# Optimization experiments

Measured on AMD Instinct MI355X. Metric: run time of the kernel, lower is better.

## Reference

```python
import jax, jax.numpy as jnp
import numpy as np

D_MODEL = 1024
NUM_HEADS = 16
DEPTH = D_MODEL // NUM_HEADS


def setup_inputs() -> dict:
    key = jax.random.key(0)
    ks = jax.random.split(key, 6)
    B, S = 2, 2048
    scale = 1.0 / np.sqrt(D_MODEL)
    return {
        "q": jax.random.normal(ks[0], (B, S, D_MODEL), jnp.float32),
        "k": jax.random.normal(ks[1], (B, S, D_MODEL), jnp.float32),
        "v": jax.random.normal(ks[2], (B, S, D_MODEL), jnp.float32),
        "wq": jax.random.normal(ks[3], (D_MODEL, D_MODEL), jnp.float32) * scale,
        "wk": jax.random.normal(ks[4], (D_MODEL, D_MODEL), jnp.float32) * scale,
        "wv": jax.random.normal(ks[5], (D_MODEL, D_MODEL), jnp.float32) * scale,
    }


def reference(q, k, v, wq, wk, wv):
    B, S, _ = q.shape
    # Linear projections (nn.Linear: x @ W.T), then split heads -> [B,H,S,depth]
    def split(x):
        return x.reshape(B, -1, NUM_HEADS, DEPTH).transpose(0, 2, 1, 3)
    Q = split(q @ wq.T)
    K = split(k @ wk.T)
    V = split(v @ wv.T)
    scores = jnp.einsum("bhqd,bhkd->bhqk", Q, K) / np.sqrt(DEPTH).astype(np.float32)
    attn = jax.nn.softmax(scores, axis=-1)
    out = jnp.einsum("bhqk,bhkd->bhqd", attn, V)
    # merge heads; note: original forward never applies self.dense
    return out.transpose(0, 2, 1, 3).reshape(B, S, D_MODEL)
```

## Files before the change

### kernel.cpp

```cpp
#include <hip/hip_runtime.h>
#include <hip/hip_bf16.h>
#include <stdint.h>

#define B_SZ 2
#define S_LEN 2048
#define DM 1024
#define NH 16
#define DEPTH 64
#define M_ROWS (B_SZ * S_LEN)
#define SCALE_Q 0.1803368801111144f

typedef __attribute__((ext_vector_type(8))) short bf16x8;
typedef __attribute__((ext_vector_type(4))) float f32x4;
typedef __attribute__((ext_vector_type(16))) float f32x16;

__device__ __forceinline__ unsigned short f2bf(float x) {
    union { float f; unsigned u; } a; a.f = x;
    unsigned r = a.u + 0x7FFF + ((a.u >> 16) & 1);
    return (unsigned short)(r >> 16);
}

__device__ __forceinline__ bf16x8 u4_to_bf8(uint4 u) {
    union { uint4 a; bf16x8 b; } c; c.a = u; return c.b;
}

__device__ __forceinline__ unsigned cvtpk_bf16(float lo, float hi) {
    unsigned r;
    asm("v_cvt_pk_bf16_f32 %0, %1, %2" : "=v"(r) : "v"(lo), "v"(hi));
    return r;
}

__device__ __forceinline__ void permswap32(unsigned &a, unsigned &b) {
    auto r = __builtin_amdgcn_permlane32_swap(a, b, false, false);
    a = r[0]; b = r[1];
}

__device__ __forceinline__ void async_ld16(const unsigned short* g, void* l) {
    __builtin_amdgcn_global_load_lds(
        (const __attribute__((address_space(1))) void*)g,
        (__attribute__((address_space(3))) void*)l,
        16, 0, 0);
}


__global__ __launch_bounds__(256)
void convert_kernel(const float* __restrict__ q, const float* __restrict__ k,
                    const float* __restrict__ v, const float* __restrict__ wq,
                    const float* __restrict__ wk, const float* __restrict__ wv,
                    unsigned short* __restrict__ dst) {
    const int z = blockIdx.y;
    const float* src = (z == 0) ? q : (z == 1) ? k : (z == 2) ? v
                     : (z == 3) ? wq : (z == 4) ? wk : wv;
    const size_t n4  = (z < 3) ? ((size_t)M_ROWS * DM / 4) : ((size_t)DM * DM / 4);
    const size_t off = (z < 3) ? ((size_t)z * M_ROWS * DM)
                               : ((size_t)3 * M_ROWS * DM + (size_t)(z - 3) * DM * DM);
    unsigned short* d = dst + off;
    const size_t stride = (size_t)gridDim.x * blockDim.x;
    for (size_t i = (size_t)blockIdx.x * blockDim.x + threadIdx.x; i < n4; i += stride) {
        float4 x = ((const float4*)src)[i];
        ushort4 p;
        p.x = f2bf(x.x); p.y = f2bf(x.y); p.z = f2bf(x.z); p.w = f2bf(x.w);
        ((ushort4*)d)[i] = p;
    }
}

__global__ __launch_bounds__(256)
void proj_gemm3_kernel(const unsigned short* __restrict__ Xall,
                       const unsigned short* __restrict__ Wall,
                       unsigned short* __restrict__ Call,
                       unsigned short* __restrict__ Vtp) {
    __shared__ unsigned short SMEM[4 * 128 * 64];

    const int z = blockIdx.z;
    const unsigned short* X = Xall + (size_t)z * M_ROWS * DM;
    const unsigned short* W = Wall + (size_t)z * DM * DM;
    unsigned short* C = Call + (size_t)z * M_ROWS * DM;

    const int tid  = threadIdx.x;
    const int wave = tid >> 6;
    const int lane = tid & 63;
    const int l32  = lane & 31;
    const int s    = lane >> 5;
    const int m0 = blockIdx.x * 128;
    const int n0 = blockIdx.y * 128;
    const int wm = (wave >> 1) * 64;
    const int wn = (wave & 1) * 64;

    const int r8 = lane >> 3;
    const int sc = (lane & 7) ^ r8;

    f32x16 acc[2][2];
#pragma unroll
    for (int mi = 0; mi < 2; ++mi)
#pragma unroll
        for (int ni = 0; ni < 2; ++ni)
#pragma unroll
            for (int r = 0; r < 16; ++r) acc[mi][ni][r] = 0.f;

#pragma unroll
    for (int i = 0; i < 4; ++i) {
        const int r = i * 32 + wave * 8 + r8;
        async_ld16(X + (size_t)(m0 + r) * DM + sc * 8,
                   (char*)SMEM + i * 4096 + wave * 1024);
        async_ld16(W + (size_t)(n0 + r) * DM + sc * 8,
                   (char*)SMEM + 32768 + i * 4096 + wave * 1024);
    }

    for (int kk = 0; kk < 16; ++kk) {
        const int cb = kk & 1;

        asm volatile("s_waitcnt vmcnt(0) lgkmcnt(0)" ::: "memory");
        __syncthreads();

        if (kk < 15) {
            const int k0 = (kk + 1) * 64;
            char* ad = (char*)SMEM + (cb ^ 1) * 16384;
            char* bd = (char*)SMEM + 32768 + (cb ^ 1) * 16384;
#pragma unroll
            for (int i = 0; i < 4; ++i) {
                const int r = i * 32 + wave * 8 + r8;
                async_ld16(X + (size_t)(m0 + r) * DM + k0 + sc * 8,
                           ad + i * 4096 + wave * 1024);
                async_ld16(W + (size_t)(n0 + r) * DM + k0 + sc * 8,
                           bd + i * 4096 + wave * 1024);
            }
        }

        const unsigned short* As = SMEM + cb * 8192;
        const unsigned short* Bs = SMEM + 16384 + cb * 8192;

#pragma unroll
        for (int ch = 0; ch < 4; ++ch) {
            bf16x8 af[2], bfr[2];
#pragma unroll
            for (int mi = 0; mi < 2; ++mi) {
                const int row = wm + mi * 32 + l32;
                af[mi] = *(const bf16x8*)&As[row * 64 + (((2 * ch + s) ^ (row & 7)) * 8)];
            }
#pragma unroll
            for (int ni = 0; ni < 2; ++ni) {
                const int row = wn + ni * 32 + l32;
                bfr[ni] = *(const bf16x8*)&Bs[row * 64 + (((2 * ch + s) ^ (row & 7)) * 8)];
            }
#pragma unroll
            for (int mi = 0; mi < 2; ++mi)
#pragma unroll
                for (int ni = 0; ni < 2; ++ni)
                    acc[mi][ni] = __builtin_amdgcn_mfma_f32_32x32x16_bf16(
                        af[mi], bfr[ni], acc[mi][ni], 0, 0, 0);
        }
    }

    if (z < 2) {
        const float scale = (z == 0) ? SCALE_Q : 1.0f;
#pragma unroll
        for (int mi = 0; mi < 2; ++mi)
#pragma unroll
            for (int ni = 0; ni < 2; ++ni)
#pragma unroll
                for (int r = 0; r < 16; ++r) {
                    const int row = m0 + wm + mi * 32 + (r & 3) + 8 * (r >> 2) + 4 * s;
                    const int col = n0 + wn + ni * 32 + l32;
                    C[(size_t)row * DM + col] = f2bf(acc[mi][ni][r] * scale);
                }
    } else {
        const int b2  = m0 >> 11;
        const int h2  = (n0 + wn) >> 6;
        const int t0l = (m0 & 2047) + wm;
        unsigned short* Tr = SMEM + (wave >> 1) * 16384 + (wave & 1) * 2368;
        const int d_sub = lane >> 3;
        const int tc    = lane & 7;
        unsigned short* VtH =
            Vtp + (size_t)((b2 * NH + h2) * DEPTH) * S_LEN;
#pragma unroll
        for (int ni = 0; ni < 2; ++ni) {
#pragma unroll
            for (int mi = 0; mi < 2; ++mi)
#pragma unroll
                for (int r = 0; r < 16; ++r) {
                    const int tl = mi * 32 + (r & 3) + 8 * (r >> 2) + 4 * s;
                    Tr[tl * 37 + l32] = f2bf(acc[mi][ni][r]);
                }
            asm volatile("s_waitcnt lgkmcnt(0)" ::: "memory");
            __builtin_amdgcn_sched_barrier(0);
#pragma unroll
            for (int di = 0; di < 4; ++di) {
                const int dl = d_sub + di * 8;
                unsigned short tmp[8];
#pragma unroll
                for (int j = 0; j < 8; ++j)
                    tmp[j] = Tr[(tc * 8 + j) * 37 + dl];
                *(bf16x8*)&VtH[(size_t)(ni * 32 + dl) * S_LEN + t0l + tc * 8] =
                    *(const bf16x8*)tmp;
            }
            asm volatile("s_waitcnt lgkmcnt(0)" ::: "memory");
            __builtin_amdgcn_sched_barrier(0);
        }
    }
}

__global__ __launch_bounds__(256, 4)
void attn8_kernel(const unsigned short* __restrict__ Qp,
                  const unsigned short* __restrict__ Kp,
                  const unsigned short* __restrict__ Vt,
                  float* __restrict__ out,
                  float* __restrict__ Op1,
                  float* __restrict__ lp) {
    __shared__ __align__(16) char smem[32768];
    unsigned short* Ks = (unsigned short*)smem;
    unsigned short* Vs = (unsigned short*)(smem + 16384);

    const int tid  = threadIdx.x;
    const int w    = tid >> 6;
    const int lane = tid & 63;
    const int l32  = lane & 31;
    const int s    = lane >> 5;
    const int r8   = lane >> 3;
    const int sc   = (lane & 7) ^ r8;

    const int lin = blockIdx.x + (blockIdx.y << 4) + (blockIdx.z << 8);
    const int v   = ((lin & 7) << 7) + (lin >> 3);
    const int qt  = v & 15;
    const int h   = (v >> 4) & 15;
    const int z   = v >> 8;

    const int q0 = qt * 128 + w * 32;
    const int b     = z >> 1;
    const int split = z & 1;
    const int tbase = split * 1024;

    const unsigned short* Kg = Kp + (size_t)(b * S_LEN + tbase) * DM + h * DEPTH;
    const unsigned short* Vg = Vt + (size_t)((b * NH + h) * DEPTH) * S_LEN + tbase;
    float* obase = split ? Op1 : out;
    float* lbase = lp + (size_t)split * M_ROWS * NH;

    bf16x8 qf[4];
    {
        const unsigned short* p =
            Qp + (size_t)(b * S_LEN + q0 + l32) * DM + h * DEPTH;
#pragma unroll
        for (int ch = 0; ch < 4; ++ch)
            qf[ch] = *(const bf16x8*)(p + ch * 16 + s * 8);
    }

    f32x16 oacc[2];
    float lacc = 0.f;
#pragma unroll
    for (int db = 0; db < 2; ++db)
#pragma unroll
        for (int r = 0; r < 16; ++r) oacc[db][r] = 0.f;

#pragma unroll
    for (int i = 0; i < 2; ++i) {
        async_ld16(Kg + (size_t)(w * 16 + i * 8 + r8) * DM + sc * 8,
                   (char*)smem + w * 2048 + i * 1024);
        async_ld16(Vg + (size_t)(w * 16 + i * 8 + r8) * S_LEN + sc * 8,
                   (char*)smem + 16384 + w * 2048 + i * 1024);
    }

    for (int it = 0; it < 16; ++it) {
        const int cb = it & 1;

        asm volatile("s_waitcnt vmcnt(0) lgkmcnt(0)" ::: "memory");
        __syncthreads();

        if (it < 15) {
            const int tn = (it + 1) * 64;
            char* kd = (char*)smem + (cb ^ 1) * 8192 + w * 2048;
            char* vd = (char*)smem + 16384 + (cb ^ 1) * 8192 + w * 2048;
#pragma unroll
            for (int i = 0; i < 2; ++i) {
                async_ld16(Kg + (size_t)(tn + w * 16 + i * 8 + r8) * DM + sc * 8,
                           kd + i * 1024);
                async_ld16(Vg + (size_t)(w * 16 + i * 8 + r8) * S_LEN + tn + sc * 8,
                           vd + i * 1024);
            }
        }

        const unsigned short* Kb = Ks + cb * 4096;
        const unsigned short* Vb = Vs + cb * 4096;

        f32x16 sv0, sv1;
#pragma unroll
        for (int r = 0; r < 16; ++r) { sv0[r] = 0.f; sv1[r] = 0.f; }
        __builtin_amdgcn_s_setprio(1);
#pragma unroll
        for (int ch = 0; ch < 4; ++ch) {
            bf16x8 kf0 = *(const bf16x8*)
                &Kb[l32 * 64 + (((2 * ch + s) ^ (l32 & 7)) * 8)];
            bf16x8 kf1 = *(const bf16x8*)
                &Kb[2048 + l32 * 64 + (((2 * ch + s) ^ (l32 & 7)) * 8)];
            sv0 = __builtin_amdgcn_mfma_f32_32x32x16_bf16(kf0, qf[ch], sv0, 0, 0, 0);
            sv1 = __builtin_amdgcn_mfma_f32_32x32x16_bf16(kf1, qf[ch], sv1, 0, 0, 0);
        }
        __builtin_amdgcn_s_setprio(0);

        unsigned pw[2][8];
#pragma unroll
        for (int th = 0; th < 2; ++th) {
            float p[16];
#pragma unroll
            for (int r = 0; r < 16; ++r)
                p[r] = __builtin_amdgcn_exp2f(th ? sv1[r] : sv0[r]);
            lacc += ((p[0] + p[1]) + (p[2] + p[3]))
                  + ((p[4] + p[5]) + (p[6] + p[7]))
                  + ((p[8] + p[9]) + (p[10] + p[11]))
                  + ((p[12] + p[13]) + (p[14] + p[15]));
            unsigned a0 = cvtpk_bf16(p[0],  p[1]);
            unsigned b0 = cvtpk_bf16(p[4],  p[5]);
            unsigned a1 = cvtpk_bf16(p[2],  p[3]);
            unsigned b1 = cvtpk_bf16(p[6],  p[7]);
            unsigned a2 = cvtpk_bf16(p[8],  p[9]);
            unsigned b2 = cvtpk_bf16(p[12], p[13]);
            unsigned a3 = cvtpk_bf16(p[10], p[11]);
            unsigned b3 = cvtpk_bf16(p[14], p[15]);
            permswap32(a0, b0);
            permswap32(a1, b1);
            permswap32(a2, b2);
            permswap32(a3, b3);
            pw[th][0] = a0; pw[th][1] = a1; pw[th][2] = b0; pw[th][3] = b1;
            pw[th][4] = a2; pw[th][5] = a3; pw[th][6] = b2; pw[th][7] = b3;
        }

#pragma unroll
        for (int th = 0; th < 2; ++th) {
            const int vcb = th * 4;
#pragma unroll
            for (int ch = 0; ch < 2; ++ch) {
                uint4 pu;
                pu.x = pw[th][ch * 4 + 0];
                pu.y = pw[th][ch * 4 + 1];
                pu.z = pw[th][ch * 4 + 2];
                pu.w = pw[th][ch * 4 + 3];
                bf16x8 pf = u4_to_bf8(pu);
                __builtin_amdgcn_s_setprio(1);
#pragma unroll
                for (int db = 0; db < 2; ++db) {
                    const int drow = db * 32 + l32;
                    bf16x8 vf = *(const bf16x8*)
                        &Vb[drow * 64 + (((vcb + 2 * ch + s) ^ (l32 & 7)) * 8)];
                    oacc[db] = __builtin_amdgcn_mfma_f32_32x32x16_bf16(
                        vf, pf, oacc[db], 0, 0, 0);
                }
                __builtin_amdgcn_s_setprio(0);
            }
        }
    }

    asm volatile("s_waitcnt vmcnt(0)" ::: "memory");

    const float l0 = lacc + __shfl_xor(lacc, 32, 64);
    if (s == 0)
        lbase[(size_t)(b * S_LEN + q0 + l32) * NH + h] = l0;

    __syncthreads();
    float* Of = (float*)(smem + w * 4608);
#pragma unroll
    for (int c = 0; c < 2; ++c) {
        if ((l32 >> 4) == c) {
            const int qh = l32 & 15;
#pragma unroll
            for (int db = 0; db < 2; ++db)
#pragma unroll
                for (int m = 0; m < 4; ++m) {
                    float4 v4;
                    v4.x = oacc[db][4 * m + 0];
                    v4.y = oacc[db][4 * m + 1];
                    v4.z = oacc[db][4 * m + 2];
                    v4.w = oacc[db][4 * m + 3];
                    *(float4*)&Of[qh * 68 + db * 32 + 8 * m + 4 * s] = v4;
                }
        }
        asm volatile("" ::: "memory");
#pragma unroll
        for (int i = 0; i < 4; ++i) {
            const int row = i * 4 + (lane >> 4);
            const int c4 = lane & 15;
            float4 v4 = *(const float4*)&Of[row * 68 + c4 * 4];
            *(float4*)&obase[(size_t)(b * S_LEN + q0 + c * 16 + row) * DM
                             + h * DEPTH + c4 * 4] = v4;
        }
        asm volatile("" ::: "memory");
    }
}

__global__ __launch_bounds__(256)
void combine_kernel(float* __restrict__ out, const float* __restrict__ Op1,
                    const float* __restrict__ lp) {
    const int i4 = blockIdx.x * 256 + threadIdx.x;
    const int row = i4 >> 8;
    const int c4  = i4 & 255;
    const int h   = c4 >> 4;
    const float l = lp[row * NH + h] + lp[M_ROWS * NH + row * NH + h];
    const float inv = 1.0f / l;
    float4 a = ((const float4*)out)[i4];
    float4 bq = ((const float4*)Op1)[i4];
    a.x = (a.x + bq.x) * inv;
    a.y = (a.y + bq.y) * inv;
    a.z = (a.z + bq.z) * inv;
    a.w = (a.w + bq.w) * inv;
    ((float4*)out)[i4] = a;
}

#define LDK 72

__global__ __launch_bounds__(256)
void proj_gemm_kernel(const float* __restrict__ q, const float* __restrict__ k,
                      const float* __restrict__ v, const float* __restrict__ wq,
                      const float* __restrict__ wk, const float* __restrict__ wv,
                      unsigned short* __restrict__ Qp, unsigned short* __restrict__ Kp,
                      unsigned short* __restrict__ Vp) {
    __shared__ unsigned short As[128 * LDK];
    __shared__ unsigned short Bs[128 * LDK];

    const int z = blockIdx.z;
    const float* __restrict__ X = (z == 0) ? q : (z == 1) ? k : v;
    const float* __restrict__ W = (z == 0) ? wq : (z == 1) ? wk : wv;
    unsigned short* __restrict__ C = (z == 0) ? Qp : (z == 1) ? Kp : Vp;

    const int tid  = threadIdx.x;
    const int wave = tid >> 6;
    const int lane = tid & 63;
    const int quad = lane >> 4;
    const int l16  = lane & 15;
    const int m0 = blockIdx.x * 128;
    const int n0 = blockIdx.y * 128;
    const int wm = (wave >> 1) * 64;
    const int wn = (wave & 1) * 64;

    f32x4 acc[4][4];
#pragma unroll
    for (int mt = 0; mt < 4; ++mt)
#pragma unroll
        for (int nt = 0; nt < 4; ++nt)
            acc[mt][nt] = (f32x4){0.f, 0.f, 0.f, 0.f};

    for (int k0 = 0; k0 < DM; k0 += 64) {
#pragma unroll
        for (int vv = 0; vv < 8; ++vv) {
            int vecid = tid + 256 * vv;
            int r  = vecid >> 4;
            int c4 = vecid & 15;
            const float4 xa = *(const float4*)&X[(size_t)(m0 + r) * DM + k0 + c4 * 4];
            ushort4 pa;
            pa.x = f2bf(xa.x); pa.y = f2bf(xa.y); pa.z = f2bf(xa.z); pa.w = f2bf(xa.w);
            *(ushort4*)&As[r * LDK + c4 * 4] = pa;
            const float4 xb = *(const float4*)&W[(size_t)(n0 + r) * DM + k0 + c4 * 4];
            ushort4 pb;
            pb.x = f2bf(xb.x); pb.y = f2bf(xb.y); pb.z = f2bf(xb.z); pb.w = f2bf(xb.w);
            *(ushort4*)&Bs[r * LDK + c4 * 4] = pb;
        }
        __syncthreads();

#pragma unroll
        for (int kc = 0; kc < 2; ++kc) {
            bf16x8 af[4], bfr[4];
#pragma unroll
            for (int mt = 0; mt < 4; ++mt)
                af[mt] = *(const bf16x8*)&As[(wm + mt * 16 + l16) * LDK + kc * 32 + quad * 8];
#pragma unroll
            for (int nt = 0; nt < 4; ++nt)
                bfr[nt] = *(const bf16x8*)&Bs[(wn + nt * 16 + l16) * LDK + kc * 32 + quad * 8];
#pragma unroll
            for (int mt = 0; mt < 4; ++mt)
#pragma unroll
                for (int nt = 0; nt < 4; ++nt)
                    acc[mt][nt] = __builtin_amdgcn_mfma_f32_16x16x32_bf16(
                        af[mt], bfr[nt], acc[mt][nt], 0, 0, 0);
        }
        __syncthreads();
    }

#pragma unroll
    for (int mt = 0; mt < 4; ++mt)
#pragma unroll
        for (int nt = 0; nt < 4; ++nt)
#pragma unroll
            for (int r = 0; r < 4; ++r) {
                int row = m0 + wm + mt * 16 + quad * 4 + r;
                int col = n0 + wn + nt * 16 + l16;
                C[(size_t)row * DM + col] = f2bf(acc[mt][nt][r]);
            }
}

__global__ __launch_bounds__(256)
void attn_kernel(const unsigned short* __restrict__ Qp,
                 const unsigned short* __restrict__ Kp,
                 const unsigned short* __restrict__ Vp,
                 float* __restrict__ out) {
    __shared__ unsigned short Ks[64 * LDK];
    __shared__ unsigned short Vtl[64 * LDK];
    __shared__ unsigned short Ps[4 * 16 * LDK];

    const int tid  = threadIdx.x;
    const int wave = tid >> 6;
    const int lane = tid & 63;
    const int quad = lane >> 4;
    const int l16  = lane & 15;
    const int q0 = blockIdx.x * 64;
    const int h  = blockIdx.y;
    const int b  = blockIdx.z;
    const int wbase = wave * 16 * LDK;

    bf16x8 qf[2];
    {
        size_t row = (size_t)b * S_LEN + q0 + wave * 16 + l16;
        const unsigned short* p = Qp + row * DM + h * DEPTH;
        qf[0] = *(const bf16x8*)(p + quad * 8);
        qf[1] = *(const bf16x8*)(p + 32 + quad * 8);
    }

    float m_i[4], l_i[4];
    f32x4 accO[4];
#pragma unroll
    for (int r = 0; r < 4; ++r) { m_i[r] = -1e30f; l_i[r] = 0.f; }
#pragma unroll
    for (int f = 0; f < 4; ++f) accO[f] = (f32x4){0.f, 0.f, 0.f, 0.f};

    for (int t0 = 0; t0 < S_LEN; t0 += 64) {
#pragma unroll
        for (int vv = 0; vv < 2; ++vv) {
            int vecid = tid + 256 * vv;
            int r  = vecid >> 3;
            int cv = vecid & 7;
            size_t grow = (size_t)(b * S_LEN + t0 + r) * DM + h * DEPTH + cv * 8;
            *(bf16x8*)&Ks[r * LDK + cv * 8] = *(const bf16x8*)(Kp + grow);
            bf16x8 vvv = *(const bf16x8*)(Vp + grow);
#pragma unroll
            for (int j = 0; j < 8; ++j)
                Vtl[(cv * 8 + j) * LDK + r] = ((const unsigned short*)&vvv)[j];
        }
        __syncthreads();

        f32x4 sc4[4];
#pragma unroll
        for (int nt = 0; nt < 4; ++nt) {
            f32x4 a = (f32x4){0.f, 0.f, 0.f, 0.f};
            bf16x8 kf0 = *(const bf16x8*)&Ks[(nt * 16 + l16) * LDK + quad * 8];
            bf16x8 kf1 = *(const bf16x8*)&Ks[(nt * 16 + l16) * LDK + 32 + quad * 8];
            a = __builtin_amdgcn_mfma_f32_16x16x32_bf16(qf[0], kf0, a, 0, 0, 0);
            a = __builtin_amdgcn_mfma_f32_16x16x32_bf16(qf[1], kf1, a, 0, 0, 0);
            sc4[nt] = a;
        }
#pragma unroll
        for (int nt = 0; nt < 4; ++nt)
#pragma unroll
            for (int r = 0; r < 4; ++r) sc4[nt][r] *= 0.125f;

#pragma unroll
        for (int r = 0; r < 4; ++r) {
            float mx = fmaxf(fmaxf(sc4[0][r], sc4[1][r]), fmaxf(sc4[2][r], sc4[3][r]));
#pragma unroll
            for (int off = 1; off < 16; off <<= 1)
                mx = fmaxf(mx, __shfl_xor(mx, off, 64));
            float mnew = fmaxf(m_i[r], mx);
            float alpha = __expf(m_i[r] - mnew);
            float rs = 0.f;
#pragma unroll
            for (int nt = 0; nt < 4; ++nt) {
                float p = __expf(sc4[nt][r] - mnew);
                sc4[nt][r] = p;
                rs += p;
            }
#pragma unroll
            for (int off = 1; off < 16; off <<= 1)
                rs += __shfl_xor(rs, off, 64);
            l_i[r] = l_i[r] * alpha + rs;
            m_i[r] = mnew;
#pragma unroll
            for (int f = 0; f < 4; ++f) accO[f][r] *= alpha;
        }

#pragma unroll
        for (int nt = 0; nt < 4; ++nt)
#pragma unroll
            for (int r = 0; r < 4; ++r)
                Ps[wbase + (quad * 4 + r) * LDK + nt * 16 + l16] = f2bf(sc4[nt][r]);
        __syncthreads();

        bf16x8 pf0 = *(const bf16x8*)&Ps[wbase + l16 * LDK + quad * 8];
        bf16x8 pf1 = *(const bf16x8*)&Ps[wbase + l16 * LDK + 32 + quad * 8];
#pragma unroll
        for (int f = 0; f < 4; ++f) {
            bf16x8 vf0 = *(const bf16x8*)&Vtl[(f * 16 + l16) * LDK + quad * 8];
            bf16x8 vf1 = *(const bf16x8*)&Vtl[(f * 16 + l16) * LDK + 32 + quad * 8];
            accO[f] = __builtin_amdgcn_mfma_f32_16x16x32_bf16(pf0, vf0, accO[f], 0, 0, 0);
            accO[f] = __builtin_amdgcn_mfma_f32_16x16x32_bf16(pf1, vf1, accO[f], 0, 0, 0);
        }
        __syncthreads();
    }

#pragma unroll
    for (int f = 0; f < 4; ++f)
#pragma unroll
        for (int r = 0; r < 4; ++r) {
            size_t row = (size_t)b * S_LEN + q0 + wave * 16 + quad * 4 + r;
            out[row * DM + h * DEPTH + f * 16 + l16] = accO[f][r] / l_i[r];
        }
}

extern "C" void kernel_launch(void* const* d_in, const int* in_sizes, int n_in,
                              void* d_out, int out_size, void* d_ws, size_t ws_size,
                              hipStream_t stream) {
    const float* q  = (const float*)d_in[0];
    const float* k  = (const float*)d_in[1];
    const float* v  = (const float*)d_in[2];
    const float* wq = (const float*)d_in[3];
    const float* wk = (const float*)d_in[4];
    const float* wv = (const float*)d_in[5];
    float* out = (float*)d_out;

    unsigned short* ws = (unsigned short*)d_ws;
    const size_t NPROJ = (size_t)M_ROWS * DM;
    const size_t NW    = (size_t)DM * DM;

    const size_t need = (3 * NPROJ + 3 * NW + 3 * NPROJ) * sizeof(unsigned short);

    if (ws_size >= need) {
        unsigned short* Xbf = ws;
        unsigned short* Wbf = ws + 3 * NPROJ;
        unsigned short* Cp  = ws + 3 * NPROJ + 3 * NW;
        unsigned short* Qp  = Cp;
        unsigned short* Kp  = Cp + NPROJ;
        unsigned short* Vt  = Cp + 2 * NPROJ;
        float*          Op1 = (float*)(ws + NPROJ);
        float*          lp  = (float*)(ws + 3 * NPROJ);

        convert_kernel<<<dim3(256, 6), 256, 0, stream>>>(q, k, v, wq, wk, wv, Xbf);
        proj_gemm3_kernel<<<dim3(M_ROWS / 128, DM / 128, 3), 256, 0, stream>>>(
            Xbf, Wbf, Cp, Vt);
        attn8_kernel<<<dim3(S_LEN / 128, NH, 4), 256, 0, stream>>>(
            Qp, Kp, Vt, out, Op1, lp);
        combine_kernel<<<dim3(M_ROWS * DM / 4 / 256), 256, 0, stream>>>(out, Op1, lp);
    } else {
        unsigned short* Qp = ws;
        unsigned short* Kp = ws + NPROJ;
        unsigned short* Vp = ws + 2 * NPROJ;
        proj_gemm_kernel<<<dim3(M_ROWS / 128, DM / 128, 3), 256, 0, stream>>>(
            q, k, v, wq, wk, wv, Qp, Kp, Vp);
        attn_kernel<<<dim3(S_LEN / 64, NH, B_SZ), 256, 0, stream>>>(Qp, Kp, Vp, out);
    }
}
```

Before: 186.5 us.

## Split KV across warp pairs in-block and fold combine into attention kernel

Result: faster. 182.8 us (-2.0%).

```diff
diff --git a/kernel.cpp b/kernel.cpp
--- a/kernel.cpp
+++ b/kernel.cpp
@@ -203,44 +203,38 @@
 void attn8_kernel(const unsigned short* __restrict__ Qp,
                   const unsigned short* __restrict__ Kp,
                   const unsigned short* __restrict__ Vt,
-                  float* __restrict__ out,
-                  float* __restrict__ Op1,
-                  float* __restrict__ lp) {
+                  float* __restrict__ out) {
     __shared__ __align__(16) char smem[32768];
     unsigned short* Ks = (unsigned short*)smem;
     unsigned short* Vs = (unsigned short*)(smem + 16384);
 
     const int tid  = threadIdx.x;
     const int w    = tid >> 6;
+    const int p    = w >> 1;
     const int lane = tid & 63;
     const int l32  = lane & 31;
     const int s    = lane >> 5;
     const int r8   = lane >> 3;
     const int sc   = (lane & 7) ^ r8;
 
-    const int lin = blockIdx.x + (blockIdx.y << 4) + (blockIdx.z << 8);
+    const int lin = blockIdx.x + (blockIdx.y << 5) + (blockIdx.z << 9);
     const int v   = ((lin & 7) << 7) + (lin >> 3);
-    const int qt  = v & 15;
-    const int h   = (v >> 4) & 15;
-    const int z   = v >> 8;
-
-    const int q0 = qt * 128 + w * 32;
-    const int b     = z >> 1;
-    const int split = z & 1;
-    const int tbase = split * 1024;
-
-    const unsigned short* Kg = Kp + (size_t)(b * S_LEN + tbase) * DM + h * DEPTH;
-    const unsigned short* Vg = Vt + (size_t)((b * NH + h) * DEPTH) * S_LEN + tbase;
-    float* obase = split ? Op1 : out;
-    float* lbase = lp + (size_t)split * M_ROWS * NH;
+    const int qt  = v & 31;
+    const int h   = (v >> 5) & 15;
+    const int b   = v >> 9;
+
+    const int q0 = qt * 64 + (w & 1) * 32;
+
+    const unsigned short* Kg = Kp + (size_t)(b * S_LEN) * DM + h * DEPTH;
+    const unsigned short* Vg = Vt + (size_t)((b * NH + h) * DEPTH) * S_LEN;
 
     bf16x8 qf[4];
     {
-        const unsigned short* p =
+        const unsigned short* pq =
             Qp + (size_t)(b * S_LEN + q0 + l32) * DM + h * DEPTH;
 #pragma unroll
         for (int ch = 0; ch < 4; ++ch)
-            qf[ch] = *(const bf16x8*)(p + ch * 16 + s * 8);
+            qf[ch] = *(const bf16x8*)(pq + ch * 16 + s * 8);
     }
 
     f32x16 oacc[2];
@@ -252,27 +246,31 @@
 
 #pragma unroll
     for (int i = 0; i < 2; ++i) {
-        async_ld16(Kg + (size_t)(w * 16 + i * 8 + r8) * DM + sc * 8,
+        async_ld16(Kg + (size_t)(p * 1024 + (w & 1) * 16 + i * 8 + r8) * DM + sc * 8,
                    (char*)smem + w * 2048 + i * 1024);
-        async_ld16(Vg + (size_t)(w * 16 + i * 8 + r8) * S_LEN + sc * 8,
+        const int cc = sc;
+        const int keyoff = (cc >> 2) * 1024 + (cc & 3) * 8;
+        async_ld16(Vg + (size_t)(w * 16 + i * 8 + r8) * S_LEN + keyoff,
                    (char*)smem + 16384 + w * 2048 + i * 1024);
     }
 
-    for (int it = 0; it < 16; ++it) {
+    for (int it = 0; it < 32; ++it) {
         const int cb = it & 1;
 
         asm volatile("s_waitcnt vmcnt(0) lgkmcnt(0)" ::: "memory");
         __syncthreads();
 
-        if (it < 15) {
-            const int tn = (it + 1) * 64;
+        if (it < 31) {
+            const int tn = (it + 1) * 32;
             char* kd = (char*)smem + (cb ^ 1) * 8192 + w * 2048;
             char* vd = (char*)smem + 16384 + (cb ^ 1) * 8192 + w * 2048;
 #pragma unroll
             for (int i = 0; i < 2; ++i) {
-                async_ld16(Kg + (size_t)(tn + w * 16 + i * 8 + r8) * DM + sc * 8,
+                async_ld16(Kg + (size_t)(p * 1024 + tn + (w & 1) * 16 + i * 8 + r8) * DM + sc * 8,
                            kd + i * 1024);
-                async_ld16(Vg + (size_t)(w * 16 + i * 8 + r8) * S_LEN + tn + sc * 8,
+                const int cc = sc;
+                const int keyoff = (cc >> 2) * 1024 + tn + (cc & 3) * 8;
+                async_ld16(Vg + (size_t)(w * 16 + i * 8 + r8) * S_LEN + keyoff,
                            vd + i * 1024);
             }
         }
@@ -280,126 +278,127 @@
         const unsigned short* Kb = Ks + cb * 4096;
         const unsigned short* Vb = Vs + cb * 4096;
 
-        f32x16 sv0, sv1;
-#pragma unroll
-        for (int r = 0; r < 16; ++r) { sv0[r] = 0.f; sv1[r] = 0.f; }
+        f32x16 sv;
+#pragma unroll
+        for (int r = 0; r < 16; ++r) sv[r] = 0.f;
         __builtin_amdgcn_s_setprio(1);
 #pragma unroll
         for (int ch = 0; ch < 4; ++ch) {
-            bf16x8 kf0 = *(const bf16x8*)
-                &Kb[l32 * 64 + (((2 * ch + s) ^ (l32 & 7)) * 8)];
-            bf16x8 kf1 = *(const bf16x8*)
-                &Kb[2048 + l32 * 64 + (((2 * ch + s) ^ (l32 & 7)) * 8)];
-            sv0 = __builtin_amdgcn_mfma_f32_32x32x16_bf16(kf0, qf[ch], sv0, 0, 0, 0);
-            sv1 = __builtin_amdgcn_mfma_f32_32x32x16_bf16(kf1, qf[ch], sv1, 0, 0, 0);
+            bf16x8 kf = *(const bf16x8*)
+                &Kb[(p * 32 + l32) * 64 + (((2 * ch + s) ^ (l32 & 7)) * 8)];
+            sv = __builtin_amdgcn_mfma_f32_32x32x16_bf16(kf, qf[ch], sv, 0, 0, 0);
         }
         __builtin_amdgcn_s_setprio(0);
 
-        unsigned pw[2][8];
-#pragma unroll
-        for (int th = 0; th < 2; ++th) {
-            float p[16];
+        float pr[16];
+#pragma unroll
+        for (int r = 0; r < 16; ++r)
+            pr[r] = __builtin_amdgcn_exp2f(sv[r]);
+        lacc += ((pr[0] + pr[1]) + (pr[2] + pr[3]))
+              + ((pr[4] + pr[5]) + (pr[6] + pr[7]))
+              + ((pr[8] + pr[9]) + (pr[10] + pr[11]))
+              + ((pr[12] + pr[13]) + (pr[14] + pr[15]));
+        unsigned a0 = cvtpk_bf16(pr[0],  pr[1]);
+        unsigned b0 = cvtpk_bf16(pr[4],  pr[5]);
+        unsigned a1 = cvtpk_bf16(pr[2],  pr[3]);
+        unsigned b1 = cvtpk_bf16(pr[6],  pr[7]);
+        unsigned a2 = cvtpk_bf16(pr[8],  pr[9]);
+        unsigned b2 = cvtpk_bf16(pr[12], pr[13]);
+        unsigned a3 = cvtpk_bf16(pr[10], pr[11]);
+        unsigned b3 = cvtpk_bf16(pr[14], pr[15]);
+        permswap32(a0, b0);
+        permswap32(a1, b1);
+        permswap32(a2, b2);
+        permswap32(a3, b3);
+        unsigned pw[8];
+        pw[0] = a0; pw[1] = a1; pw[2] = b0; pw[3] = b1;
+        pw[4] = a2; pw[5] = a3; pw[6] = b2; pw[7] = b3;
+
+#pragma unroll
+        for (int ch = 0; ch < 2; ++ch) {
+            uint4 pu;
+            pu.x = pw[ch * 4 + 0];
+            pu.y = pw[ch * 4 + 1];
+            pu.z = pw[ch * 4 + 2];
+            pu.w = pw[ch * 4 + 3];
+            bf16x8 pf = u4_to_bf8(pu);
+            __builtin_amdgcn_s_setprio(1);
+#pragma unroll
+            for (int db = 0; db < 2; ++db) {
+                const int drow = db * 32 + l32;
+                bf16x8 vf = *(const bf16x8*)
+                    &Vb[drow * 64 + (((p * 4 + 2 * ch + s) ^ (l32 & 7)) * 8)];
+                oacc[db] = __builtin_amdgcn_mfma_f32_32x32x16_bf16(
+                    vf, pf, oacc[db], 0, 0, 0);
+            }
+            __builtin_amdgcn_s_setprio(0);
+        }
+    }
+
+    asm volatile("s_waitcnt vmcnt(0)" ::: "memory");
+    __syncthreads();
+
+    float* Ex = (float*)smem;
+    if (w >= 2) {
+        float* dst = Ex + (w - 2) * 2048;
+#pragma unroll
+        for (int db = 0; db < 2; ++db)
 #pragma unroll
             for (int r = 0; r < 16; ++r)
-                p[r] = __builtin_amdgcn_exp2f(th ? sv1[r] : sv0[r]);
-            lacc += ((p[0] + p[1]) + (p[2] + p[3]))
-                  + ((p[4] + p[5]) + (p[6] + p[7]))
-                  + ((p[8] + p[9]) + (p[10] + p[11]))
-                  + ((p[12] + p[13]) + (p[14] + p[15]));
-            unsigned a0 = cvtpk_bf16(p[0],  p[1]);
-            unsigned b0 = cvtpk_bf16(p[4],  p[5]);
-            unsigned a1 = cvtpk_bf16(p[2],  p[3]);
-            unsigned b1 = cvtpk_bf16(p[6],  p[7]);
-            unsigned a2 = cvtpk_bf16(p[8],  p[9]);
-            unsigned b2 = cvtpk_bf16(p[12], p[13]);
-            unsigned a3 = cvtpk_bf16(p[10], p[11]);
-            unsigned b3 = cvtpk_bf16(p[14], p[15]);
-            permswap32(a0, b0);
-            permswap32(a1, b1);
-            permswap32(a2, b2);
-            permswap32(a3, b3);
-            pw[th][0] = a0; pw[th][1] = a1; pw[th][2] = b0; pw[th][3] = b1;
-            pw[th][4] = a2; pw[th][5] = a3; pw[th][6] = b2; pw[th][7] = b3;
-        }
-
-#pragma unroll
-        for (int th = 0; th < 2; ++th) {
-            const int vcb = th * 4;
-#pragma unroll
-            for (int ch = 0; ch < 2; ++ch) {
-                uint4 pu;
-                pu.x = pw[th][ch * 4 + 0];
-                pu.y = pw[th][ch * 4 + 1];
-                pu.z = pw[th][ch * 4 + 2];
-                pu.w = pw[th][ch * 4 + 3];
-                bf16x8 pf = u4_to_bf8(pu);
-                __builtin_amdgcn_s_setprio(1);
-#pragma unroll
-                for (int db = 0; db < 2; ++db) {
-                    const int drow = db * 32 + l32;
-                    bf16x8 vf = *(const bf16x8*)
-                        &Vb[drow * 64 + (((vcb + 2 * ch + s) ^ (l32 & 7)) * 8)];
-                    oacc[db] = __builtin_amdgcn_mfma_f32_32x32x16_bf16(
-                        vf, pf, oacc[db], 0, 0, 0);
-                }
-                __builtin_amdgcn_s_setprio(0);
-            }
-        }
-    }
-
-    asm volatile("s_waitcnt vmcnt(0)" ::: "memory");
-
-    const float l0 = lacc + __shfl_xor(lacc, 32, 64);
-    if (s == 0)
-        lbase[(size_t)(b * S_LEN + q0 + l32) * NH + h] = l0;
-
+                dst[(db * 16 + r) * 64 + lane] = oacc[db][r];
+        Ex[4096 + (w - 2) * 64 + lane] = lacc;
+    }
+    asm volatile("s_waitcnt lgkmcnt(0)" ::: "memory");
     __syncthreads();
-    float* Of = (float*)(smem + w * 4608);
-#pragma unroll
-    for (int c = 0; c < 2; ++c) {
-        if ((l32 >> 4) == c) {
-            const int qh = l32 & 15;
-#pragma unroll
-            for (int db = 0; db < 2; ++db)
-#pragma unroll
-                for (int m = 0; m < 4; ++m) {
-                    float4 v4;
-                    v4.x = oacc[db][4 * m + 0];
-                    v4.y = oacc[db][4 * m + 1];
-                    v4.z = oacc[db][4 * m + 2];
-                    v4.w = oacc[db][4 * m + 3];
-                    *(float4*)&Of[qh * 68 + db * 32 + 8 * m + 4 * s] = v4;
-                }
-        }
-        asm volatile("" ::: "memory");
-#pragma unroll
-        for (int i = 0; i < 4; ++i) {
-            const int row = i * 4 + (lane >> 4);
-            const int c4 = lane & 15;
-            float4 v4 = *(const float4*)&Of[row * 68 + c4 * 4];
-            *(float4*)&obase[(size_t)(b * S_LEN + q0 + c * 16 + row) * DM
-                             + h * DEPTH + c4 * 4] = v4;
-        }
-        asm volatile("" ::: "memory");
-    }
-}
-
-__global__ __launch_bounds__(256)
-void combine_kernel(float* __restrict__ out, const float* __restrict__ Op1,
-                    const float* __restrict__ lp) {
-    const int i4 = blockIdx.x * 256 + threadIdx.x;
-    const int row = i4 >> 8;
-    const int c4  = i4 & 255;
-    const int h   = c4 >> 4;
-    const float l = lp[row * NH + h] + lp[M_ROWS * NH + row * NH + h];
-    const float inv = 1.0f / l;
-    float4 a = ((const float4*)out)[i4];
-    float4 bq = ((const float4*)Op1)[i4];
-    a.x = (a.x + bq.x) * inv;
-    a.y = (a.y + bq.y) * inv;
-    a.z = (a.z + bq.z) * inv;
-    a.w = (a.w + bq.w) * inv;
-    ((float4*)out)[i4] = a;
+
+    if (w < 2) {
+        float* src = Ex + w * 2048;
+#pragma unroll
+        for (int db = 0; db < 2; ++db)
+#pragma unroll
+            for (int r = 0; r < 16; ++r)
+                oacc[db][r] += src[(db * 16 + r) * 64 + lane];
+        lacc += Ex[4096 + w * 64 + lane];
+        const float lt = lacc + __shfl_xor(lacc, 32, 64);
+        const float inv = 1.0f / lt;
+        if (s == 0) Ex[4224 + w * 32 + l32] = inv;
+        asm volatile("s_waitcnt lgkmcnt(0)" ::: "memory");
+        __builtin_amdgcn_sched_barrier(0);
+
+        float* Of = (float*)(smem + 18432 + w * 4608);
+#pragma unroll
+        for (int c = 0; c < 2; ++c) {
+            if ((l32 >> 4) == c) {
+                const int qh = l32 & 15;
+#pragma unroll
+                for (int db = 0; db < 2; ++db)
+#pragma unroll
+                    for (int m = 0; m < 4; ++m) {
+                        float4 v4;
+                        v4.x = oacc[db][4 * m + 0];
+                        v4.y = oacc[db][4 * m + 1];
+                        v4.z = oacc[db][4 * m + 2];
+                        v4.w = oacc[db][4 * m + 3];
+                        *(float4*)&Of[qh * 68 + db * 32 + 8 * m + 4 * s] = v4;
+                    }
+            }
+            asm volatile("s_waitcnt lgkmcnt(0)" ::: "memory");
+            __builtin_amdgcn_sched_barrier(0);
+#pragma unroll
+            for (int i = 0; i < 4; ++i) {
+                const int row = i * 4 + (lane >> 4);
+                const int c4 = lane & 15;
+                float4 v4 = *(const float4*)&Of[row * 68 + c4 * 4];
+                const float iv = Ex[4224 + w * 32 + c * 16 + row];
+                v4.x *= iv; v4.y *= iv; v4.z *= iv; v4.w *= iv;
+                *(float4*)&out[(size_t)(b * S_LEN + q0 - (w & 1) * 32
+                                        + (w & 1) * 32 + c * 16 + row) * DM
+                               + h * DEPTH + c4 * 4] = v4;
+            }
+            asm volatile("s_waitcnt lgkmcnt(0)" ::: "memory");
+            __builtin_amdgcn_sched_barrier(0);
+        }
+    }
 }
 
 #define LDK 72
@@ -623,15 +622,12 @@
         unsigned short* Qp  = Cp;
         unsigned short* Kp  = Cp + NPROJ;
         unsigned short* Vt  = Cp + 2 * NPROJ;
-        float*          Op1 = (float*)(ws + NPROJ);
-        float*          lp  = (float*)(ws + 3 * NPROJ);
 
         convert_kernel<<<dim3(256, 6), 256, 0, stream>>>(q, k, v, wq, wk, wv, Xbf);
         proj_gemm3_kernel<<<dim3(M_ROWS / 128, DM / 128, 3), 256, 0, stream>>>(
             Xbf, Wbf, Cp, Vt);
-        attn8_kernel<<<dim3(S_LEN / 128, NH, 4), 256, 0, stream>>>(
-            Qp, Kp, Vt, out, Op1, lp);
-        combine_kernel<<<dim3(M_ROWS * DM / 4 / 256), 256, 0, stream>>>(out, Op1, lp);
+        attn8_kernel<<<dim3(S_LEN / 64, NH, B_SZ), 256, 0, stream>>>(
+            Qp, Kp, Vt, out);
     } else {
         unsigned short* Qp = ws;
         unsigned short* Kp = ws + NPROJ;
```
